# Kernel tuning notes

Measured on AMD Instinct MI355X. Metric: run time of the kernel, lower is better.

The kernel has to match this reference:

```python
import jax, jax.numpy as jnp
import numpy as np

D = 512       # d_model
H = 8         # n_heads per pathway MHA
CTX_H = 2     # router context_attention heads
P = 16        # num_attention_pathways
K = 8         # top_k_pathways
B = 8
S = 1024
TEMP = 1.0
RH1, RH2 = 128, 64  # router hidden sizes


def mha(x, in_w, in_b, out_w, out_b, n_heads):
    """torch.nn.MultiheadAttention (batch_first, eval mode, no mask)."""
    b, s, d = x.shape
    dh = d // n_heads
    qkv = x @ in_w.T + in_b                      # [b,s,3d]
    q, k, v = jnp.split(qkv, 3, axis=-1)
    sh = lambda t: t.reshape(b, s, n_heads, dh).transpose(0, 2, 1, 3)
    q, k, v = sh(q), sh(k), sh(v)
    scale = 1.0 / float(np.sqrt(dh))
    attn = jax.nn.softmax(jnp.einsum('bhqd,bhkd->bhqk', q, k) * scale, axis=-1)
    o = jnp.einsum('bhqk,bhkd->bhqd', attn, v).transpose(0, 2, 1, 3).reshape(b, s, d)
    return o @ out_w.T + out_b


def setup_inputs() -> dict:
    key = jax.random.key(0)
    ks = jax.random.split(key, 16)
    w = 0.05  # weight init scale to keep attention logits sane
    return {
        'x': jax.random.normal(ks[0], (B, S, D), jnp.float32),
        'ctx_in_w': jax.random.normal(ks[1], (3 * D, D), jnp.float32) * w,
        'ctx_in_b': jnp.zeros((3 * D,), jnp.float32),
        'ctx_out_w': jax.random.normal(ks[2], (D, D), jnp.float32) * w,
        'ctx_out_b': jnp.zeros((D,), jnp.float32),
        'r_w1': jax.random.normal(ks[3], (RH1, D), jnp.float32) * w,
        'r_b1': jnp.zeros((RH1,), jnp.float32),
        'r_w2': jax.random.normal(ks[4], (RH2, RH1), jnp.float32) * w,
        'r_b2': jnp.zeros((RH2,), jnp.float32),
        'r_w3': jax.random.normal(ks[5], (P, RH2), jnp.float32) * w,
        'r_b3': jnp.zeros((P,), jnp.float32),
        'p_in_w': jax.random.normal(ks[6], (P, 3 * D, D), jnp.float32) * w,
        'p_in_b': jnp.zeros((P, 3 * D), jnp.float32),
        'p_out_w': jax.random.normal(ks[7], (P, D, D), jnp.float32) * w,
        'p_out_b': jnp.zeros((P, D), jnp.float32),
    }


def reference(x, ctx_in_w, ctx_in_b, ctx_out_w, ctx_out_b,
              r_w1, r_b1, r_w2, r_b2, r_w3, r_b3,
              p_in_w, p_in_b, p_out_w, p_out_b):
    b, s, d = x.shape
    # --- SemanticPathwayRouter ---
    attended = mha(x, ctx_in_w, ctx_in_b, ctx_out_w, ctx_out_b, CTX_H)
    h = jax.nn.relu(attended @ r_w1.T + r_b1)
    h = jax.nn.relu(h @ r_w2.T + r_b2)
    pathway_scores = h @ r_w3.T + r_b3            # [b,s,P]
    # --- GLBL load-balance loss (eval: no buffer updates) ---
    probs_lb = jax.nn.softmax(pathway_scores, axis=-1)
    freq = probs_lb.mean(axis=(0, 1))             # [P] (frequencies == avg scores)
    glbl_loss = P * jnp.sum(freq * freq)
    # --- top-k gating: softmax -> topk scatter -> renormalize ---
    probs = jax.nn.softmax(pathway_scores / TEMP, axis=-1)
    top_v, top_i = jax.lax.top_k(probs, K)        # [b,s,K]
    bi = jnp.arange(b)[:, None, None]
    si = jnp.arange(s)[None, :, None]
    weights = jnp.zeros_like(probs).at[bi, si, top_i].set(top_v)
    weights = weights / (weights.sum(axis=-1, keepdims=True) + 1e-8)
    # --- combine: weighted sum of P full-MHA experts (scan keeps memory low) ---
    wp = jnp.moveaxis(weights, -1, 0)             # [P,b,s]
    def step(acc, params):
        iw, ib, ow, ob, wk = params
        return acc + mha(x, iw, ib, ow, ob, H) * wk[..., None], None
    output, _ = jax.lax.scan(step, jnp.zeros_like(x),
                             (p_in_w, p_in_b, p_out_w, p_out_b, wp))
    return output, glbl_loss, weights
```

## Files before the change

kernel.cpp:

```cpp
#include <hip/hip_runtime.h>
#include <math.h>

#define TOKENS 8192
#define DM 512
#define TD 1536
#define SEQ 1024
#define NPATH 16
#define TOPK 8

typedef __bf16 bf16x8v __attribute__((ext_vector_type(8)));
typedef __bf16 bf16x4v __attribute__((ext_vector_type(4)));
typedef float f32x4v __attribute__((ext_vector_type(4)));

__device__ __forceinline__ void gload_lds16(const void* gp, unsigned lds_byte_off) {
    __builtin_amdgcn_global_load_lds(
        (const __attribute__((address_space(1))) unsigned int*)(uintptr_t)gp,
        (__attribute__((address_space(3))) unsigned int*)(uintptr_t)lds_byte_off,
        16, 0, 0);
}

__global__ __launch_bounds__(256)
void gemm_f32_nt(const float* __restrict__ A, const float* __restrict__ B,
                 const float* __restrict__ bias, float* __restrict__ C,
                 int M, int N, int K, int lda, int ldb, int ldc,
                 float alpha, int relu, int zmode)
{
    __shared__ float As[16][132];
    __shared__ float Bs[16][132];
    if (zmode == 1) {
        const int z = blockIdx.z, bb = z >> 1, hh = z & 1;
        A += (size_t)bb * SEQ * TD + hh * 256;
        B += (size_t)bb * SEQ * TD + 512 + hh * 256;
        C += (size_t)z * SEQ * SEQ;
    }
    const int tid = threadIdx.x;
    const int bm = blockIdx.y << 7, bn = blockIdx.x << 7;
    const int tx4 = (tid & 15) << 2, ty4 = ((tid >> 4) & 15) << 2;
    float acc[8][8] = {};
    for (int k0 = 0; k0 < K; k0 += 16) {
        __syncthreads();
#pragma unroll
        for (int it = 0; it < 2; ++it) {
            const int u = (it << 8) + tid;
            const int row = u >> 2, kc4 = (u & 3) << 2;
            const float4 av = *(const float4*)(A + (size_t)(bm + row) * lda + k0 + kc4);
            As[kc4 + 0][row] = av.x; As[kc4 + 1][row] = av.y;
            As[kc4 + 2][row] = av.z; As[kc4 + 3][row] = av.w;
            const float4 bv = *(const float4*)(B + (size_t)(bn + row) * ldb + k0 + kc4);
            Bs[kc4 + 0][row] = bv.x; Bs[kc4 + 1][row] = bv.y;
            Bs[kc4 + 2][row] = bv.z; Bs[kc4 + 3][row] = bv.w;
        }
        __syncthreads();
#pragma unroll
        for (int kk = 0; kk < 16; ++kk) {
            const float4 a0 = *(const float4*)&As[kk][ty4];
            const float4 a1 = *(const float4*)&As[kk][64 + ty4];
            const float4 b0 = *(const float4*)&Bs[kk][tx4];
            const float4 b1 = *(const float4*)&Bs[kk][64 + tx4];
            const float aa[8] = {a0.x, a0.y, a0.z, a0.w, a1.x, a1.y, a1.z, a1.w};
            const float bb[8] = {b0.x, b0.y, b0.z, b0.w, b1.x, b1.y, b1.z, b1.w};
#pragma unroll
            for (int i = 0; i < 8; ++i)
#pragma unroll
                for (int j = 0; j < 8; ++j)
                    acc[i][j] = fmaf(aa[i], bb[j], acc[i][j]);
        }
    }
    float bcol[8] = {};
    if (bias) {
        const float4 bL = *(const float4*)(bias + bn + tx4);
        const float4 bH = *(const float4*)(bias + bn + 64 + tx4);
        bcol[0] = bL.x; bcol[1] = bL.y; bcol[2] = bL.z; bcol[3] = bL.w;
        bcol[4] = bH.x; bcol[5] = bH.y; bcol[6] = bH.z; bcol[7] = bH.w;
    }
#pragma unroll
    for (int i = 0; i < 8; ++i) {
        const int row = bm + ((i < 4) ? (ty4 + i) : (64 + ty4 + i - 4));
        float* cp = C + (size_t)row * ldc + bn;
        float v[8];
#pragma unroll
        for (int j = 0; j < 8; ++j) {
            v[j] = alpha * acc[i][j] + bcol[j];
            if (relu) v[j] = fmaxf(v[j], 0.f);
        }
        *(float4*)(cp + tx4) = make_float4(v[0], v[1], v[2], v[3]);
        *(float4*)(cp + 64 + tx4) = make_float4(v[4], v[5], v[6], v[7]);
    }
}

__global__ __launch_bounds__(256)
void gemm_f32_pv(const float* __restrict__ Sb, const float* __restrict__ qkv,
                 float* __restrict__ obuf)
{
    __shared__ float As[16][132];
    __shared__ float Bs[16][128];
    const int z = blockIdx.z, bb = z >> 1, hh = z & 1;
    const float* A = Sb + (size_t)z * SEQ * SEQ;
    const float* B = qkv + (size_t)bb * SEQ * TD + 1024 + hh * 256;
    float* C = obuf + (size_t)bb * SEQ * 512 + hh * 256;
    const int tid = threadIdx.x;
    const int bm = blockIdx.y << 7, bn = blockIdx.x << 7;
    const int tx4 = (tid & 15) << 2, ty4 = ((tid >> 4) & 15) << 2;
    float acc[8][8] = {};
    for (int k0 = 0; k0 < SEQ; k0 += 16) {
        __syncthreads();
#pragma unroll
        for (int it = 0; it < 2; ++it) {
            const int u = (it << 8) + tid;
            const int row = u >> 2, kc4 = (u & 3) << 2;
            const float4 av = *(const float4*)(A + (size_t)(bm + row) * SEQ + k0 + kc4);
            As[kc4 + 0][row] = av.x; As[kc4 + 1][row] = av.y;
            As[kc4 + 2][row] = av.z; As[kc4 + 3][row] = av.w;
            const int krow = u >> 5, n4 = (u & 31) << 2;
            *(float4*)&Bs[krow][n4] = *(const float4*)(B + (size_t)(k0 + krow) * TD + bn + n4);
        }
        __syncthreads();
#pragma unroll
        for (int kk = 0; kk < 16; ++kk) {
            const float4 a0 = *(const float4*)&As[kk][ty4];
            const float4 a1 = *(const float4*)&As[kk][64 + ty4];
            const float4 b0 = *(const float4*)&Bs[kk][tx4];
            const float4 b1 = *(const float4*)&Bs[kk][64 + tx4];
            const float aa[8] = {a0.x, a0.y, a0.z, a0.w, a1.x, a1.y, a1.z, a1.w};
            const float bb[8] = {b0.x, b0.y, b0.z, b0.w, b1.x, b1.y, b1.z, b1.w};
#pragma unroll
            for (int i = 0; i < 8; ++i)
#pragma unroll
                for (int j = 0; j < 8; ++j)
                    acc[i][j] = fmaf(aa[i], bb[j], acc[i][j]);
        }
    }
#pragma unroll
    for (int i = 0; i < 8; ++i) {
        const int row = bm + ((i < 4) ? (ty4 + i) : (64 + ty4 + i - 4));
        float* cp = C + (size_t)row * 512 + bn;
        *(float4*)(cp + tx4) = make_float4(acc[i][0], acc[i][1], acc[i][2], acc[i][3]);
        *(float4*)(cp + 64 + tx4) = make_float4(acc[i][4], acc[i][5], acc[i][6], acc[i][7]);
    }
}

__global__ __launch_bounds__(256)
void softmax_rows(float* __restrict__ S_)
{
    const int row = blockIdx.x * 4 + (threadIdx.x >> 6);
    const int lane = threadIdx.x & 63;
    float* rp = S_ + (size_t)row * 1024 + lane * 16;
    float4 v[4];
#pragma unroll
    for (int i = 0; i < 4; ++i) v[i] = *(const float4*)(rp + i * 4);
    float mx = -INFINITY;
#pragma unroll
    for (int i = 0; i < 4; ++i)
        mx = fmaxf(mx, fmaxf(fmaxf(v[i].x, v[i].y), fmaxf(v[i].z, v[i].w)));
#pragma unroll
    for (int off = 1; off < 64; off <<= 1) mx = fmaxf(mx, __shfl_xor(mx, off));
    float sum = 0.f;
#pragma unroll
    for (int i = 0; i < 4; ++i) {
        v[i].x = __expf(v[i].x - mx); v[i].y = __expf(v[i].y - mx);
        v[i].z = __expf(v[i].z - mx); v[i].w = __expf(v[i].w - mx);
        sum += v[i].x + v[i].y + v[i].z + v[i].w;
    }
#pragma unroll
    for (int off = 1; off < 64; off <<= 1) sum += __shfl_xor(sum, off);
    const float inv = 1.f / sum;
#pragma unroll
    for (int i = 0; i < 4; ++i) {
        v[i].x *= inv; v[i].y *= inv; v[i].z *= inv; v[i].w *= inv;
        *(float4*)(rp + i * 4) = v[i];
    }
}

__global__ __launch_bounds__(256)
void gemm_f32(const float* __restrict__ A, const float* __restrict__ W,
              const float* __restrict__ bias, float* __restrict__ C,
              int M, int N, int K, int relu)
{
    __shared__ float As[16][64];
    __shared__ float Bs[16][64];
    const int bm = blockIdx.y << 6;
    const int bn = blockIdx.x << 6;
    const int tid = threadIdx.x;
    const int tx = tid & 15, ty = tid >> 4;
    const int lr = tid >> 2;
    const int lc = (tid & 3) << 2;
    float acc[4][4] = {};
    for (int k0 = 0; k0 < K; k0 += 16) {
        float4 av = *(const float4*)(A + (size_t)(bm + lr) * K + (k0 + lc));
        float4 bv = make_float4(0.f, 0.f, 0.f, 0.f);
        const int wr = bn + lr;
        if (wr < N) bv = *(const float4*)(W + (size_t)wr * K + (k0 + lc));
        __syncthreads();
        As[lc + 0][lr] = av.x; As[lc + 1][lr] = av.y;
        As[lc + 2][lr] = av.z; As[lc + 3][lr] = av.w;
        Bs[lc + 0][lr] = bv.x; Bs[lc + 1][lr] = bv.y;
        Bs[lc + 2][lr] = bv.z; Bs[lc + 3][lr] = bv.w;
        __syncthreads();
#pragma unroll
        for (int kk = 0; kk < 16; ++kk) {
            const float4 a4 = *(const float4*)(&As[kk][ty << 2]);
            const float4 b4 = *(const float4*)(&Bs[kk][tx << 2]);
            const float a[4] = {a4.x, a4.y, a4.z, a4.w};
            const float b[4] = {b4.x, b4.y, b4.z, b4.w};
#pragma unroll
            for (int i = 0; i < 4; ++i)
#pragma unroll
                for (int j = 0; j < 4; ++j)
                    acc[i][j] = fmaf(a[i], b[j], acc[i][j]);
        }
    }
#pragma unroll
    for (int i = 0; i < 4; ++i) {
        const int m = bm + (ty << 2) + i;
#pragma unroll
        for (int j = 0; j < 4; ++j) {
            const int n = bn + (tx << 2) + j;
            if (n < N) {
                float v = acc[i][j] + bias[n];
                if (relu) v = fmaxf(v, 0.f);
                C[(size_t)m * N + n] = v;
            }
        }
    }
}

template <int DH>
__global__ __launch_bounds__(256)
void flash_attn(const float* __restrict__ qkv, float* __restrict__ O,
                int H, float scale)
{
    constexpr int NU = DH / 64;
    __shared__ float Qs[32][DH + 4];
    __shared__ float Ks[32][DH + 4];
    __shared__ float Vs[32][DH + 4];
    __shared__ float Ps[32][33];
    const int tid = threadIdx.x;
    const int g2 = tid & 15;
    const int rs = tid >> 4;
    const int bh = blockIdx.y;
    const int b = bh / H, h = bh - b * H;
    const int rb = blockIdx.x << 5;
    const float* qb = qkv + (size_t)b * SEQ * TD + (size_t)h * DH;
    const float* kb = qb + DM;
    const float* vb = qb + 2 * DM;

    for (int idx = tid; idx < 32 * (DH / 4); idx += 256) {
        const int rr = idx / (DH / 4);
        const int dp = (idx - rr * (DH / 4)) << 2;
        float4 v = *(const float4*)(qb + (size_t)(rb + rr) * TD + dp);
        v.x *= scale; v.y *= scale; v.z *= scale; v.w *= scale;
        *(float4*)&Qs[rr][dp] = v;
    }
    float m0 = -INFINITY, m1 = -INFINITY, l0 = 0.f, l1 = 0.f;
    float4 o0[NU], o1[NU];
#pragma unroll
    for (int u = 0; u < NU; ++u) {
        o0[u] = make_float4(0.f, 0.f, 0.f, 0.f);
        o1[u] = make_float4(0.f, 0.f, 0.f, 0.f);
    }
    __syncthreads();

    for (int kt = 0; kt < SEQ; kt += 32) {
        for (int idx = tid; idx < 32 * (DH / 4); idx += 256) {
            const int rr = idx / (DH / 4);
            const int dp = (idx - rr * (DH / 4)) << 2;
            *(float4*)&Ks[rr][dp] = *(const float4*)(kb + (size_t)(kt + rr) * TD + dp);
            *(float4*)&Vs[rr][dp] = *(const float4*)(vb + (size_t)(kt + rr) * TD + dp);
        }
        __syncthreads();
        float s00 = 0.f, s01 = 0.f, s10 = 0.f, s11 = 0.f;
        const int cA = g2, cB = g2 + 16;
#pragma unroll 8
        for (int i = 0; i < DH; i += 4) {
            const float4 q0 = *(const float4*)&Qs[rs][i];
            const float4 q1 = *(const float4*)&Qs[rs + 16][i];
            const float4 k0 = *(const float4*)&Ks[cA][i];
            const float4 k1 = *(const float4*)&Ks[cB][i];
            s00 += q0.x * k0.x + q0.y * k0.y + q0.z * k0.z + q0.w * k0.w;
            s01 += q0.x * k1.x + q0.y * k1.y + q0.z * k1.z + q0.w * k1.w;
            s10 += q1.x * k0.x + q1.y * k0.y + q1.z * k0.z + q1.w * k0.w;
            s11 += q1.x * k1.x + q1.y * k1.y + q1.z * k1.z + q1.w * k1.w;
        }
        float ml0 = fmaxf(s00, s01), ml1 = fmaxf(s10, s11);
#pragma unroll
        for (int off = 1; off < 16; off <<= 1) {
            ml0 = fmaxf(ml0, __shfl_xor(ml0, off));
            ml1 = fmaxf(ml1, __shfl_xor(ml1, off));
        }
        const float n0 = fmaxf(m0, ml0), n1 = fmaxf(m1, ml1);
        const float f0 = __expf(m0 - n0), f1 = __expf(m1 - n1);
        const float p00 = __expf(s00 - n0), p01 = __expf(s01 - n0);
        const float p10 = __expf(s10 - n1), p11 = __expf(s11 - n1);
        float sum0 = p00 + p01, sum1 = p10 + p11;
#pragma unroll
        for (int off = 1; off < 16; off <<= 1) {
            sum0 += __shfl_xor(sum0, off);
            sum1 += __shfl_xor(sum1, off);
        }
        l0 = l0 * f0 + sum0; l1 = l1 * f1 + sum1;
        m0 = n0; m1 = n1;
#pragma unroll
        for (int u = 0; u < NU; ++u) {
            o0[u].x *= f0; o0[u].y *= f0; o0[u].z *= f0; o0[u].w *= f0;
            o1[u].x *= f1; o1[u].y *= f1; o1[u].z *= f1; o1[u].w *= f1;
        }
        Ps[rs][cA] = p00; Ps[rs][cB] = p01;
        Ps[rs + 16][cA] = p10; Ps[rs + 16][cB] = p11;
        __syncthreads();
#pragma unroll 4
        for (int c = 0; c < 32; ++c) {
            const float pv0 = Ps[rs][c];
            const float pv1 = Ps[rs + 16][c];
#pragma unroll
            for (int u = 0; u < NU; ++u) {
                const float4 v4 = *(const float4*)&Vs[c][(g2 << 2) + (u << 6)];
                o0[u].x = fmaf(pv0, v4.x, o0[u].x);
                o0[u].y = fmaf(pv0, v4.y, o0[u].y);
                o0[u].z = fmaf(pv0, v4.z, o0[u].z);
                o0[u].w = fmaf(pv0, v4.w, o0[u].w);
                o1[u].x = fmaf(pv1, v4.x, o1[u].x);
                o1[u].y = fmaf(pv1, v4.y, o1[u].y);
                o1[u].z = fmaf(pv1, v4.z, o1[u].z);
                o1[u].w = fmaf(pv1, v4.w, o1[u].w);
            }
        }
        __syncthreads();
    }
    const float i0 = 1.f / l0, i1 = 1.f / l1;
    float* ob0 = O + (size_t)b * SEQ * DM + (size_t)(rb + rs) * DM + h * DH;
    float* ob1 = ob0 + (size_t)16 * DM;
#pragma unroll
    for (int u = 0; u < NU; ++u) {
        float4 w0 = o0[u];
        w0.x *= i0; w0.y *= i0; w0.z *= i0; w0.w *= i0;
        *(float4*)(ob0 + (g2 << 2) + (u << 6)) = w0;
        float4 w1 = o1[u];
        w1.x *= i1; w1.y *= i1; w1.z *= i1; w1.w *= i1;
        *(float4*)(ob1 + (g2 << 2) + (u << 6)) = w1;
    }
}

__global__ __launch_bounds__(256)
void router_epilogue(const float* __restrict__ scores, float* __restrict__ freq,
                     float* __restrict__ weights)
{
    const int t = blockIdx.x * 256 + threadIdx.x;
    float s[NPATH];
#pragma unroll
    for (int i = 0; i < NPATH; ++i) s[i] = scores[(size_t)t * NPATH + i];
    float mx = s[0];
#pragma unroll
    for (int i = 1; i < NPATH; ++i) mx = fmaxf(mx, s[i]);
    float p[NPATH];
    float sum = 0.f;
#pragma unroll
    for (int i = 0; i < NPATH; ++i) { p[i] = expf(s[i] - mx); sum += p[i]; }
    const float inv = 1.f / sum;
#pragma unroll
    for (int i = 0; i < NPATH; ++i) p[i] *= inv;
#pragma unroll
    for (int i = 0; i < NPATH; ++i) {
        float v = p[i];
        for (int off = 32; off >= 1; off >>= 1) v += __shfl_xor(v, off);
        if ((threadIdx.x & 63) == 0) atomicAdd(&freq[i], v);
    }
    unsigned used = 0u;
    float topv[TOPK];
    int topi[TOPK];
    float wsum = 0.f;
#pragma unroll
    for (int k = 0; k < TOPK; ++k) {
        float best = -1.f; int bi = 0;
#pragma unroll
        for (int i = 0; i < NPATH; ++i) {
            if (!((used >> i) & 1u) && p[i] > best) { best = p[i]; bi = i; }
        }
        used |= 1u << bi;
        topv[k] = best; topi[k] = bi;
        wsum += best;
    }
    const float winv = 1.f / (wsum + 1e-8f);
    float w[NPATH];
#pragma unroll
    for (int i = 0; i < NPATH; ++i) w[i] = 0.f;
#pragma unroll
    for (int k = 0; k < TOPK; ++k) w[topi[k]] = topv[k] * winv;
#pragma unroll
    for (int i = 0; i < NPATH; ++i) weights[(size_t)t * NPATH + i] = w[i];
}

__global__ void glbl_loss_kernel(const float* __restrict__ freq, float* __restrict__ out)
{
    if (threadIdx.x == 0 && blockIdx.x == 0) {
        float acc = 0.f;
        for (int i = 0; i < NPATH; ++i) {
            const float f = freq[i] * (1.f / (float)TOKENS);
            acc += f * f;
        }
        out[0] = (float)NPATH * acc;
    }
}

__global__ __launch_bounds__(256)
void cast_f32_bf16(const float* __restrict__ src, __bf16* __restrict__ dst, int n)
{
    const int i = (blockIdx.x * 256 + threadIdx.x) * 4;
    if (i < n) {
        const float4 v = *(const float4*)(src + i);
        bf16x4v o;
        o[0] = (__bf16)v.x; o[1] = (__bf16)v.y; o[2] = (__bf16)v.z; o[3] = (__bf16)v.w;
        *(bf16x4v*)(dst + i) = o;
    }
}

__global__ __launch_bounds__(256)
void gemm_bf16_qkv(const __bf16* __restrict__ A, const __bf16* __restrict__ B,
                   const float* __restrict__ bias, __bf16* __restrict__ C,
                   int N, int K)
{
    __shared__ __attribute__((aligned(16))) __bf16 As[128 * 32];
    __shared__ __attribute__((aligned(16))) __bf16 Bs[128 * 32];
    const int tid = threadIdx.x;
    const int l = tid & 63, w = tid >> 6;
    const int wr = w >> 1, wc = w & 1;
    const int a16 = l & 15, g = l >> 4;
    const int bm = blockIdx.y << 7, bn = blockIdx.x << 7;
    const unsigned asA = (unsigned)(uintptr_t)(void*)&As[0];
    const unsigned asB = (unsigned)(uintptr_t)(void*)&Bs[0];

    f32x4v acc[4][4] = {};
    for (int k0 = 0; k0 < K; k0 += 32) {
        __syncthreads();
#pragma unroll
        for (int it = 0; it < 2; ++it) {
            const int u = it * 256 + tid;
            const int row = u >> 2, cc = u & 3;
            const unsigned dst = (unsigned)((it * 256 + w * 64) * 16);
            gload_lds16(A + (size_t)(bm + row) * K + k0 + cc * 8, asA + dst);
            gload_lds16(B + (size_t)(bn + row) * K + k0 + cc * 8, asB + dst);
        }
        __syncthreads();
        bf16x8v af[4], bf[4];
#pragma unroll
        for (int m = 0; m < 4; ++m)
            af[m] = *(const bf16x8v*)&As[(wr * 64 + m * 16 + a16) * 32 + g * 8];
#pragma unroll
        for (int n = 0; n < 4; ++n)
            bf[n] = *(const bf16x8v*)&Bs[(wc * 64 + n * 16 + a16) * 32 + g * 8];
#pragma unroll
        for (int m = 0; m < 4; ++m)
#pragma unroll
            for (int n = 0; n < 4; ++n)
                acc[m][n] = __builtin_amdgcn_mfma_f32_16x16x32_bf16(af[m], bf[n], acc[m][n], 0, 0, 0);
    }
#pragma unroll
    for (int n = 0; n < 4; ++n) {
        const int col = bn + wc * 64 + n * 16 + a16;
        const float bv = bias[col];
        const float sc = (col < DM) ? 0.125f : 1.0f;
#pragma unroll
        for (int m = 0; m < 4; ++m) {
            const int row0 = bm + wr * 64 + m * 16 + g * 4;
#pragma unroll
            for (int r = 0; r < 4; ++r)
                C[(size_t)(row0 + r) * N + col] = (__bf16)((acc[m][n][r] + bv) * sc);
        }
    }
}

__global__ __launch_bounds__(256)
void gemm_bf16_out(const __bf16* __restrict__ A, const __bf16* __restrict__ B,
                   const float* __restrict__ bias, const float* __restrict__ wts,
                   float* __restrict__ out, int path, int first)
{
    __shared__ __attribute__((aligned(16))) __bf16 As[128 * 32];
    __shared__ __attribute__((aligned(16))) __bf16 Bs[128 * 32];
    const int tid = threadIdx.x;
    const int l = tid & 63, w = tid >> 6;
    const int wr = w >> 1, wc = w & 1;
    const int a16 = l & 15, g = l >> 4;
    const int bm = blockIdx.y << 7, bn = blockIdx.x << 7;
    const unsigned asA = (unsigned)(uintptr_t)(void*)&As[0];
    const unsigned asB = (unsigned)(uintptr_t)(void*)&Bs[0];

    f32x4v acc[4][4] = {};
    for (int k0 = 0; k0 < DM; k0 += 32) {
        __syncthreads();
#pragma unroll
        for (int it = 0; it < 2; ++it) {
            const int u = it * 256 + tid;
            const int row = u >> 2, cc = u & 3;
            const unsigned dst = (unsigned)((it * 256 + w * 64) * 16);
            gload_lds16(A + (size_t)(bm + row) * DM + k0 + cc * 8, asA + dst);
            gload_lds16(B + (size_t)(bn + row) * DM + k0 + cc * 8, asB + dst);
        }
        __syncthreads();
        bf16x8v af[4], bf[4];
#pragma unroll
        for (int m = 0; m < 4; ++m)
            af[m] = *(const bf16x8v*)&As[(wr * 64 + m * 16 + a16) * 32 + g * 8];
#pragma unroll
        for (int n = 0; n < 4; ++n)
            bf[n] = *(const bf16x8v*)&Bs[(wc * 64 + n * 16 + a16) * 32 + g * 8];
#pragma unroll
        for (int m = 0; m < 4; ++m)
#pragma unroll
            for (int n = 0; n < 4; ++n)
                acc[m][n] = __builtin_amdgcn_mfma_f32_16x16x32_bf16(af[m], bf[n], acc[m][n], 0, 0, 0);
    }
#pragma unroll
    for (int m = 0; m < 4; ++m) {
        const int row0 = bm + wr * 64 + m * 16 + g * 4;
#pragma unroll
        for (int r = 0; r < 4; ++r) {
            const int row = row0 + r;
            const float wk = wts[(size_t)row * NPATH + path];
#pragma unroll
            for (int n = 0; n < 4; ++n) {
                const int col = bn + wc * 64 + n * 16 + a16;
                const float v = (acc[m][n][r] + bias[col]) * wk;
                const size_t oi = (size_t)row * DM + col;
                if (first) out[oi] = v; else out[oi] += v;
            }
        }
    }
}

__global__ __launch_bounds__(256)
void attn_bf16(const __bf16* __restrict__ qkv, __bf16* __restrict__ O)
{
    __shared__ __attribute__((aligned(16))) __bf16 Ks[64 * 72];
    __shared__ __attribute__((aligned(16))) __bf16 Vt[64 * 72];
    __shared__ __attribute__((aligned(16))) __bf16 Pq[4][16 * 72];
    const int tid = threadIdx.x;
    const int l = tid & 63, w = tid >> 6;
    const int a = l & 15, g = l >> 4;
    const int bh = blockIdx.y;
    const int b = bh >> 3, h = bh & 7;
    const int qb = blockIdx.x << 6;
    const size_t base = (size_t)b * SEQ * TD;

    bf16x8v qf[2];
    {
        const int qrow = qb + w * 16 + a;
        const __bf16* qp = qkv + base + (size_t)qrow * TD + h * 64 + g * 8;
        qf[0] = *(const bf16x8v*)qp;
        qf[1] = *(const bf16x8v*)(qp + 32);
    }
    float m_ = -INFINITY, l_ = 0.f;
    f32x4v o_[4] = {};
    __bf16* pw = &Pq[w][0];

    for (int kt = 0; kt < SEQ; kt += 64) {
#pragma unroll
        for (int it = 0; it < 2; ++it) {
            const int u = it * 256 + tid;
            const int kr = u >> 3, c8 = u & 7;
            const __bf16* kp = qkv + base + (size_t)(kt + kr) * TD + DM + h * 64 + c8 * 8;
            const bf16x8v kv = *(const bf16x8v*)kp;
            *(bf16x8v*)&Ks[kr * 72 + c8 * 8] = kv;
            const bf16x8v vv = *(const bf16x8v*)(kp + DM);
            const int swzg = ((kr >> 3) ^ c8) & 7;
#pragma unroll
            for (int j = 0; j < 8; ++j)
                Vt[(c8 * 8 + j) * 72 + swzg * 8 + (kr & 7)] = vv[j];
        }
        __syncthreads();

        f32x4v s[4] = {};
#pragma unroll
        for (int kc = 0; kc < 4; ++kc) {
            const bf16x8v kf0 = *(const bf16x8v*)&Ks[(kc * 16 + a) * 72 + g * 8];
            const bf16x8v kf1 = *(const bf16x8v*)&Ks[(kc * 16 + a) * 72 + 32 + g * 8];
            s[kc] = __builtin_amdgcn_mfma_f32_16x16x32_bf16(kf0, qf[0], s[kc], 0, 0, 0);
            s[kc] = __builtin_amdgcn_mfma_f32_16x16x32_bf16(kf1, qf[1], s[kc], 0, 0, 0);
        }

        float pmax = s[0][0];
#pragma unroll
        for (int kc = 0; kc < 4; ++kc)
#pragma unroll
            for (int r = 0; r < 4; ++r) pmax = fmaxf(pmax, s[kc][r]);
        pmax = fmaxf(pmax, __shfl_xor(pmax, 16));
        pmax = fmaxf(pmax, __shfl_xor(pmax, 32));

        if (__any(pmax > m_ + 8.f)) {
            const float nm = fmaxf(m_, pmax);
            const float f = __expf(m_ - nm);
            m_ = nm;
            l_ *= f;
#pragma unroll
            for (int r = 0; r < 4; ++r) {
                const float fr = __shfl(f, 4 * g + r);
#pragma unroll
                for (int dc = 0; dc < 4; ++dc) o_[dc][r] *= fr;
            }
        }
        float p[4][4];
        float lsum = 0.f;
#pragma unroll
        for (int kc = 0; kc < 4; ++kc)
#pragma unroll
            for (int r = 0; r < 4; ++r) {
                p[kc][r] = __expf(s[kc][r] - m_);
                lsum += p[kc][r];
            }
        lsum += __shfl_xor(lsum, 16);
        lsum += __shfl_xor(lsum, 32);
        l_ += lsum;

#pragma unroll
        for (int kc = 0; kc < 4; ++kc) {
            bf16x4v pk;
            pk[0] = (__bf16)p[kc][0]; pk[1] = (__bf16)p[kc][1];
            pk[2] = (__bf16)p[kc][2]; pk[3] = (__bf16)p[kc][3];
            *(bf16x4v*)&pw[a * 72 + kc * 16 + g * 4] = pk;
        }
        asm volatile("s_waitcnt lgkmcnt(0)" ::: "memory");

#pragma unroll
        for (int dc = 0; dc < 4; ++dc) {
            const int vrow = dc * 16 + a;
#pragma unroll
            for (int kh = 0; kh < 2; ++kh) {
                const bf16x8v pa = *(const bf16x8v*)&pw[a * 72 + kh * 32 + g * 8];
                const bf16x8v vf = *(const bf16x8v*)&Vt[vrow * 72 + ((((kh << 2) + g) ^ ((vrow >> 3) & 7)) & 7) * 8];
                o_[dc] = __builtin_amdgcn_mfma_f32_16x16x32_bf16(pa, vf, o_[dc], 0, 0, 0);
            }
        }
        __syncthreads();
    }

    float linv[4];
#pragma unroll
    for (int r = 0; r < 4; ++r) linv[r] = 1.f / __shfl(l_, 4 * g + r);
    const int row0 = qb + w * 16 + g * 4;
#pragma unroll
    for (int dc = 0; dc < 4; ++dc)
#pragma unroll
        for (int r = 0; r < 4; ++r)
            O[(size_t)(b * SEQ + row0 + r) * DM + h * 64 + dc * 16 + a] = (__bf16)(o_[dc][r] * linv[r]);
}

extern "C" void kernel_launch(void* const* d_in, const int* in_sizes, int n_in,
                              void* d_out, int out_size, void* d_ws, size_t ws_size,
                              hipStream_t stream)
{
    const float* x         = (const float*)d_in[0];
    const float* ctx_in_w  = (const float*)d_in[1];
    const float* ctx_in_b  = (const float*)d_in[2];
    const float* ctx_out_w = (const float*)d_in[3];
    const float* ctx_out_b = (const float*)d_in[4];
    const float* r_w1      = (const float*)d_in[5];
    const float* r_b1      = (const float*)d_in[6];
    const float* r_w2      = (const float*)d_in[7];
    const float* r_b2      = (const float*)d_in[8];
    const float* r_w3      = (const float*)d_in[9];
    const float* r_b3      = (const float*)d_in[10];
    const float* p_in_w    = (const float*)d_in[11];
    const float* p_in_b    = (const float*)d_in[12];
    const float* p_out_w   = (const float*)d_in[13];
    const float* p_out_b   = (const float*)d_in[14];

    float* out  = (float*)d_out;
    float* loss = out + (size_t)TOKENS * DM;
    float* wts  = loss + 1;

    float* F = (float*)d_ws;
    float* qkvbuf   = F;
    float* obuf     = F + 12582912;
    float* attended = F;
    float* h1       = F + 4194304;
    float* h2       = F + 5242880;
    float* scores   = F + 5767168;
    float* freq     = F + 5898240;

    const int M = TOKENS;
    dim3 blk(256);
    const bool big = ws_size >= (size_t)134217728;

    hipMemsetAsync(freq, 0, NPATH * sizeof(float), stream);
    gemm_f32_nt<<<dim3(TD / 128, M / 128), blk, 0, stream>>>(
        x, ctx_in_w, ctx_in_b, qkvbuf, M, TD, DM, DM, DM, TD, 1.f, 0, 0);
    if (big) {
        float* Sbuf = F + 16777216;
        gemm_f32_nt<<<dim3(8, 8, 16), blk, 0, stream>>>(
            qkvbuf, qkvbuf, nullptr, Sbuf, SEQ, SEQ, 256, TD, TD, SEQ, 0.0625f, 0, 1);
        softmax_rows<<<dim3(16 * SEQ / 4), blk, 0, stream>>>(Sbuf);
        gemm_f32_pv<<<dim3(2, 8, 16), blk, 0, stream>>>(Sbuf, qkvbuf, obuf);
    } else {
        flash_attn<256><<<dim3(SEQ / 32, 8 * 2), blk, 0, stream>>>(qkvbuf, obuf, 2, 1.f / 16.f);
    }
    gemm_f32_nt<<<dim3(DM / 128, M / 128), blk, 0, stream>>>(
        obuf, ctx_out_w, ctx_out_b, attended, M, DM, DM, DM, DM, DM, 1.f, 0, 0);
    gemm_f32_nt<<<dim3(1, M / 128), blk, 0, stream>>>(
        attended, r_w1, r_b1, h1, M, 128, DM, DM, DM, 128, 1.f, 1, 0);
    gemm_f32<<<dim3(1, M / 64), blk, 0, stream>>>(h1, r_w2, r_b2, h2, M, 64, 128, 1);
    gemm_f32<<<dim3(1, M / 64), blk, 0, stream>>>(h2, r_w3, r_b3, scores, M, NPATH, 64, 0);
    router_epilogue<<<dim3(TOKENS / 256), blk, 0, stream>>>(scores, freq, wts);
    glbl_loss_kernel<<<dim3(1), dim3(64), 0, stream>>>(freq, loss);

    if (big) {
        __bf16* xb       = (__bf16*)F;
        __bf16* qkv_b    = (__bf16*)(F + 2097152);
        __bf16* obuf_b   = (__bf16*)(F + 8388608);
        __bf16* wqkv_all = (__bf16*)(F + 10485760);
        __bf16* wout_all = (__bf16*)(F + 16777216);
        cast_f32_bf16<<<dim3(TOKENS * DM / 4 / 256), blk, 0, stream>>>(x, xb, TOKENS * DM);
        cast_f32_bf16<<<dim3(NPATH * TD * DM / 4 / 256), blk, 0, stream>>>(
            p_in_w, wqkv_all, NPATH * TD * DM);
        cast_f32_bf16<<<dim3(NPATH * DM * DM / 4 / 256), blk, 0, stream>>>(
            p_out_w, wout_all, NPATH * DM * DM);
        for (int p = 0; p < NPATH; ++p) {
            gemm_bf16_qkv<<<dim3(TD / 128, M / 128), blk, 0, stream>>>(
                xb, wqkv_all + (size_t)p * TD * DM, p_in_b + (size_t)p * TD, qkv_b, TD, DM);
            attn_bf16<<<dim3(SEQ / 64, 64), blk, 0, stream>>>(qkv_b, obuf_b);
            gemm_bf16_out<<<dim3(DM / 128, M / 128), blk, 0, stream>>>(
                obuf_b, wout_all + (size_t)p * DM * DM, p_out_b + (size_t)p * DM, wts, out, p, p == 0);
        }
    } else {
        __bf16* xb     = (__bf16*)F;
        __bf16* qkv_b  = (__bf16*)(F + 6000000);
        __bf16* obuf_b = (__bf16*)(F + 12582912);
        __bf16* wqkv_b = (__bf16*)(F + 12582912 + 2100000);
        __bf16* wout_b = (__bf16*)(F + 12582912 + 2500000);
        cast_f32_bf16<<<dim3(TOKENS * DM / 4 / 256), blk, 0, stream>>>(x, xb, TOKENS * DM);
        for (int p = 0; p < NPATH; ++p) {
            cast_f32_bf16<<<dim3(TD * DM / 4 / 256), blk, 0, stream>>>(
                p_in_w + (size_t)p * TD * DM, wqkv_b, TD * DM);
            cast_f32_bf16<<<dim3(DM * DM / 4 / 256), blk, 0, stream>>>(
                p_out_w + (size_t)p * DM * DM, wout_b, DM * DM);
            gemm_bf16_qkv<<<dim3(TD / 128, M / 128), blk, 0, stream>>>(
                xb, wqkv_b, p_in_b + (size_t)p * TD, qkv_b, TD, DM);
            attn_bf16<<<dim3(SEQ / 64, 64), blk, 0, stream>>>(qkv_b, obuf_b);
            gemm_bf16_out<<<dim3(DM / 128, M / 128), blk, 0, stream>>>(
                obuf_b, wout_b, p_out_b + (size_t)p * DM, wts, out, p, p == 0);
        }
    }
}
```

Before: 2.358 ms.

## Write V transposed from QKV GEMM and load K/V fragments directly from global

The QKV GEMM epilogue now writes V into a separate per-(batch,head) transposed buffer, so the attention kernel can load K and V MFMA fragments straight from global memory into registers. This removes the LDS staging, the scalar transpose scatter into LDS and both block-wide barriers per key tile. The attention grid is also remapped to a 1D launch that groups query blocks of the same batch/head, and s_setprio is raised around the MFMA sections. The trade-offs are uncoalesced scattered stores of V in the GEMM epilogue, redundant global loads of K/V by each wave (relying on cache), and moved workspace offsets.

```diff
diff --git a/kernel.cpp b/kernel.cpp
--- a/kernel.cpp
+++ b/kernel.cpp
@@ -416,7 +416,7 @@
 __global__ __launch_bounds__(256)
 void gemm_bf16_qkv(const __bf16* __restrict__ A, const __bf16* __restrict__ B,
                    const float* __restrict__ bias, __bf16* __restrict__ C,
-                   int N, int K)
+                   __bf16* __restrict__ vT, int N, int K)
 {
     __shared__ __attribute__((aligned(16))) __bf16 As[128 * 32];
     __shared__ __attribute__((aligned(16))) __bf16 Bs[128 * 32];
@@ -457,13 +457,26 @@
     for (int n = 0; n < 4; ++n) {
         const int col = bn + wc * 64 + n * 16 + a16;
         const float bv = bias[col];
-        const float sc = (col < DM) ? 0.125f : 1.0f;
-#pragma unroll
-        for (int m = 0; m < 4; ++m) {
-            const int row0 = bm + wr * 64 + m * 16 + g * 4;
-#pragma unroll
-            for (int r = 0; r < 4; ++r)
-                C[(size_t)(row0 + r) * N + col] = (__bf16)((acc[m][n][r] + bv) * sc);
+        if (col < 1024) {
+            const float sc = (col < DM) ? 0.125f : 1.0f;
+#pragma unroll
+            for (int m = 0; m < 4; ++m) {
+                const int row0 = bm + wr * 64 + m * 16 + g * 4;
+#pragma unroll
+                for (int r = 0; r < 4; ++r)
+                    C[(size_t)(row0 + r) * N + col] = (__bf16)((acc[m][n][r] + bv) * sc);
+            }
+        } else {
+#pragma unroll
+            for (int m = 0; m < 4; ++m) {
+                const int row0 = bm + wr * 64 + m * 16 + g * 4;
+#pragma unroll
+                for (int r = 0; r < 4; ++r) {
+                    const int row = row0 + r;
+                    vT[((size_t)(row >> 10) * 512 + (col - 1024)) * SEQ + (row & 1023)] =
+                        (__bf16)(acc[m][n][r] + bv);
+                }
+            }
         }
     }
 }
@@ -527,17 +540,18 @@
 }
 
 __global__ __launch_bounds__(256)
-void attn_bf16(const __bf16* __restrict__ qkv, __bf16* __restrict__ O)
-{
-    __shared__ __attribute__((aligned(16))) __bf16 Ks[64 * 72];
-    __shared__ __attribute__((aligned(16))) __bf16 Vt[64 * 72];
+void attn_bf16(const __bf16* __restrict__ qkv, const __bf16* __restrict__ vT,
+               __bf16* __restrict__ O)
+{
     __shared__ __attribute__((aligned(16))) __bf16 Pq[4][16 * 72];
     const int tid = threadIdx.x;
     const int l = tid & 63, w = tid >> 6;
     const int a = l & 15, g = l >> 4;
-    const int bh = blockIdx.y;
+    const int i = blockIdx.x;
+    const int k = i >> 3;
+    const int bh = (i & 7) + ((k >> 4) << 3);
+    const int qb = (k & 15) << 6;
     const int b = bh >> 3, h = bh & 7;
-    const int qb = blockIdx.x << 6;
     const size_t base = (size_t)b * SEQ * TD;
 
     bf16x8v qf[2];
@@ -547,34 +561,36 @@
         qf[0] = *(const bf16x8v*)qp;
         qf[1] = *(const bf16x8v*)(qp + 32);
     }
+    const __bf16* Kg = qkv + base + (size_t)a * TD + DM + h * 64 + g * 8;
+    const __bf16* Vg = vT + ((size_t)bh * 64 + a) * SEQ + g * 8;
+
     float m_ = -INFINITY, l_ = 0.f;
     f32x4v o_[4] = {};
     __bf16* pw = &Pq[w][0];
 
     for (int kt = 0; kt < SEQ; kt += 64) {
-#pragma unroll
-        for (int it = 0; it < 2; ++it) {
-            const int u = it * 256 + tid;
-            const int kr = u >> 3, c8 = u & 7;
-            const __bf16* kp = qkv + base + (size_t)(kt + kr) * TD + DM + h * 64 + c8 * 8;
-            const bf16x8v kv = *(const bf16x8v*)kp;
-            *(bf16x8v*)&Ks[kr * 72 + c8 * 8] = kv;
-            const bf16x8v vv = *(const bf16x8v*)(kp + DM);
-            const int swzg = ((kr >> 3) ^ c8) & 7;
-#pragma unroll
-            for (int j = 0; j < 8; ++j)
-                Vt[(c8 * 8 + j) * 72 + swzg * 8 + (kr & 7)] = vv[j];
-        }
-        __syncthreads();
-
+        const __bf16* kp = Kg + (size_t)kt * TD;
+        bf16x8v kf0[4], kf1[4];
+#pragma unroll
+        for (int kc = 0; kc < 4; ++kc) {
+            kf0[kc] = *(const bf16x8v*)(kp + (size_t)(kc * 16) * TD);
+            kf1[kc] = *(const bf16x8v*)(kp + (size_t)(kc * 16) * TD + 32);
+        }
+        bf16x8v vf[4][2];
+        const __bf16* vp = Vg + kt;
+#pragma unroll
+        for (int dc = 0; dc < 4; ++dc) {
+            vf[dc][0] = *(const bf16x8v*)(vp + (size_t)(dc * 16) * SEQ);
+            vf[dc][1] = *(const bf16x8v*)(vp + (size_t)(dc * 16) * SEQ + 32);
+        }
         f32x4v s[4] = {};
+        __builtin_amdgcn_s_setprio(1);
 #pragma unroll
         for (int kc = 0; kc < 4; ++kc) {
-            const bf16x8v kf0 = *(const bf16x8v*)&Ks[(kc * 16 + a) * 72 + g * 8];
-            const bf16x8v kf1 = *(const bf16x8v*)&Ks[(kc * 16 + a) * 72 + 32 + g * 8];
-            s[kc] = __builtin_amdgcn_mfma_f32_16x16x32_bf16(kf0, qf[0], s[kc], 0, 0, 0);
-            s[kc] = __builtin_amdgcn_mfma_f32_16x16x32_bf16(kf1, qf[1], s[kc], 0, 0, 0);
-        }
+            s[kc] = __builtin_amdgcn_mfma_f32_16x16x32_bf16(kf0[kc], qf[0], s[kc], 0, 0, 0);
+            s[kc] = __builtin_amdgcn_mfma_f32_16x16x32_bf16(kf1[kc], qf[1], s[kc], 0, 0, 0);
+        }
+        __builtin_amdgcn_s_setprio(0);
 
         float pmax = s[0][0];
 #pragma unroll
@@ -617,18 +633,16 @@
             *(bf16x4v*)&pw[a * 72 + kc * 16 + g * 4] = pk;
         }
         asm volatile("s_waitcnt lgkmcnt(0)" ::: "memory");
-
+        const bf16x8v pa0 = *(const bf16x8v*)&pw[a * 72 + g * 8];
+        const bf16x8v pa1 = *(const bf16x8v*)&pw[a * 72 + 32 + g * 8];
+
+        __builtin_amdgcn_s_setprio(1);
 #pragma unroll
         for (int dc = 0; dc < 4; ++dc) {
-            const int vrow = dc * 16 + a;
-#pragma unroll
-            for (int kh = 0; kh < 2; ++kh) {
-                const bf16x8v pa = *(const bf16x8v*)&pw[a * 72 + kh * 32 + g * 8];
-                const bf16x8v vf = *(const bf16x8v*)&Vt[vrow * 72 + ((((kh << 2) + g) ^ ((vrow >> 3) & 7)) & 7) * 8];
-                o_[dc] = __builtin_amdgcn_mfma_f32_16x16x32_bf16(pa, vf, o_[dc], 0, 0, 0);
-            }
-        }
-        __syncthreads();
+            o_[dc] = __builtin_amdgcn_mfma_f32_16x16x32_bf16(pa0, vf[dc][0], o_[dc], 0, 0, 0);
+            o_[dc] = __builtin_amdgcn_mfma_f32_16x16x32_bf16(pa1, vf[dc][1], o_[dc], 0, 0, 0);
+        }
+        __builtin_amdgcn_s_setprio(0);
     }
 
     float linv[4];
@@ -674,6 +688,10 @@
     float* h2       = F + 5242880;
     float* scores   = F + 5767168;
     float* freq     = F + 5898240;
+    __bf16* xb     = (__bf16*)F;
+    __bf16* qkv_b  = (__bf16*)(F + 2097152);
+    __bf16* obuf_b = (__bf16*)(F + 8388608);
+    __bf16* vT_b   = (__bf16*)(F + 10485760);
 
     const int M = TOKENS;
     dim3 blk(256);
@@ -700,39 +718,32 @@
     router_epilogue<<<dim3(TOKENS / 256), blk, 0, stream>>>(scores, freq, wts);
     glbl_loss_kernel<<<dim3(1), dim3(64), 0, stream>>>(freq, loss);
 
+    cast_f32_bf16<<<dim3(TOKENS * DM / 4 / 256), blk, 0, stream>>>(x, xb, TOKENS * DM);
     if (big) {
-        __bf16* xb       = (__bf16*)F;
-        __bf16* qkv_b    = (__bf16*)(F + 2097152);
-        __bf16* obuf_b   = (__bf16*)(F + 8388608);
-        __bf16* wqkv_all = (__bf16*)(F + 10485760);
-        __bf16* wout_all = (__bf16*)(F + 16777216);
-        cast_f32_bf16<<<dim3(TOKENS * DM / 4 / 256), blk, 0, stream>>>(x, xb, TOKENS * DM);
+        __bf16* wqkv_all = (__bf16*)(F + 16777216);
+        __bf16* wout_all = (__bf16*)(F + 23068672);
         cast_f32_bf16<<<dim3(NPATH * TD * DM / 4 / 256), blk, 0, stream>>>(
             p_in_w, wqkv_all, NPATH * TD * DM);
         cast_f32_bf16<<<dim3(NPATH * DM * DM / 4 / 256), blk, 0, stream>>>(
             p_out_w, wout_all, NPATH * DM * DM);
         for (int p = 0; p < NPATH; ++p) {
             gemm_bf16_qkv<<<dim3(TD / 128, M / 128), blk, 0, stream>>>(
-                xb, wqkv_all + (size_t)p * TD * DM, p_in_b + (size_t)p * TD, qkv_b, TD, DM);
-            attn_bf16<<<dim3(SEQ / 64, 64), blk, 0, stream>>>(qkv_b, obuf_b);
+                xb, wqkv_all + (size_t)p * TD * DM, p_in_b + (size_t)p * TD, qkv_b, vT_b, TD, DM);
+            attn_bf16<<<dim3(1024), blk, 0, stream>>>(qkv_b, vT_b, obuf_b);
             gemm_bf16_out<<<dim3(DM / 128, M / 128), blk, 0, stream>>>(
                 obuf_b, wout_all + (size_t)p * DM * DM, p_out_b + (size_t)p * DM, wts, out, p, p == 0);
         }
     } else {
-        __bf16* xb     = (__bf16*)F;
-        __bf16* qkv_b  = (__bf16*)(F + 6000000);
-        __bf16* obuf_b = (__bf16*)(F + 12582912);
-        __bf16* wqkv_b = (__bf16*)(F + 12582912 + 2100000);
-        __bf16* wout_b = (__bf16*)(F + 12582912 + 2500000);
-        cast_f32_bf16<<<dim3(TOKENS * DM / 4 / 256), blk, 0, stream>>>(x, xb, TOKENS * DM);
+        __bf16* wqkv_b = (__bf16*)(F + 12582912);
+        __bf16* wout_b = (__bf16*)(F + 12976128);
         for (int p = 0; p < NPATH; ++p) {
             cast_f32_bf16<<<dim3(TD * DM / 4 / 256), blk, 0, stream>>>(
                 p_in_w + (size_t)p * TD * DM, wqkv_b, TD * DM);
             cast_f32_bf16<<<dim3(DM * DM / 4 / 256), blk, 0, stream>>>(
                 p_out_w + (size_t)p * DM * DM, wout_b, DM * DM);
             gemm_bf16_qkv<<<dim3(TD / 128, M / 128), blk, 0, stream>>>(
-                xb, wqkv_b, p_in_b + (size_t)p * TD, qkv_b, TD, DM);
-            attn_bf16<<<dim3(SEQ / 64, 64), blk, 0, stream>>>(qkv_b, obuf_b);
+                xb, wqkv_b, p_in_b + (size_t)p * TD, qkv_b, vT_b, TD, DM);
+            attn_bf16<<<dim3(1024), blk, 0, stream>>>(qkv_b, vT_b, obuf_b);
             gemm_bf16_out<<<dim3(DM / 128, M / 128), blk, 0, stream>>>(
                 obuf_b, wout_b, p_out_b + (size_t)p * DM, wts, out, p, p == 0);
         }
```

After: 3.499 ms. +48.4%, slower.

## Process two query tiles per wave in bf16 attention to reuse K/V loads

Applied to the files above, without the earlier changes.

Each wave in the bf16 attention kernel now handles 32 query rows (two 16-row tiles) instead of 16, so each block covers 128 queries and loads each K/V tile from global once per 128 queries rather than once per 64. The V transpose store is rewritten to pack pairs of rows into 32-bit LDS writes, and s_setprio is raised around the MFMA sections. Workspace offsets are also reshuffled. This halves the grid to 512 blocks per pathway and doubles accumulator register use, which may reduce occupancy and parallelism.

```diff
diff --git a/kernel.cpp b/kernel.cpp
--- a/kernel.cpp
+++ b/kernel.cpp
@@ -11,6 +11,7 @@
 typedef __bf16 bf16x8v __attribute__((ext_vector_type(8)));
 typedef __bf16 bf16x4v __attribute__((ext_vector_type(4)));
 typedef float f32x4v __attribute__((ext_vector_type(4)));
+typedef unsigned short u16x8 __attribute__((ext_vector_type(8)));
 
 __device__ __forceinline__ void gload_lds16(const void* gp, unsigned lds_byte_off) {
     __builtin_amdgcn_global_load_lds(
@@ -531,25 +532,30 @@
 {
     __shared__ __attribute__((aligned(16))) __bf16 Ks[64 * 72];
     __shared__ __attribute__((aligned(16))) __bf16 Vt[64 * 72];
-    __shared__ __attribute__((aligned(16))) __bf16 Pq[4][16 * 72];
+    __shared__ __attribute__((aligned(16))) __bf16 Pq[4][32 * 72];
     const int tid = threadIdx.x;
     const int l = tid & 63, w = tid >> 6;
     const int a = l & 15, g = l >> 4;
     const int bh = blockIdx.y;
     const int b = bh >> 3, h = bh & 7;
-    const int qb = blockIdx.x << 6;
+    const int qb = blockIdx.x << 7;
     const size_t base = (size_t)b * SEQ * TD;
 
-    bf16x8v qf[2];
+    bf16x8v qA0, qA1, qB0, qB1;
     {
-        const int qrow = qb + w * 16 + a;
-        const __bf16* qp = qkv + base + (size_t)qrow * TD + h * 64 + g * 8;
-        qf[0] = *(const bf16x8v*)qp;
-        qf[1] = *(const bf16x8v*)(qp + 32);
-    }
-    float m_ = -INFINITY, l_ = 0.f;
-    f32x4v o_[4] = {};
+        const __bf16* qp = qkv + base + (size_t)(qb + w * 32 + a) * TD + h * 64 + g * 8;
+        qA0 = *(const bf16x8v*)qp;
+        qA1 = *(const bf16x8v*)(qp + 32);
+        const __bf16* qp2 = qp + (size_t)16 * TD;
+        qB0 = *(const bf16x8v*)qp2;
+        qB1 = *(const bf16x8v*)(qp2 + 32);
+    }
+    float mA = -INFINITY, lA = 0.f, mB = -INFINITY, lB = 0.f;
+    f32x4v oA[4] = {}, oB[4] = {};
     __bf16* pw = &Pq[w][0];
+    const int c8v = tid & 7;
+    const int pr  = tid >> 3;
+    const int vcol8 = (pr >> 2) ^ c8v;
 
     for (int kt = 0; kt < SEQ; kt += 64) {
 #pragma unroll
@@ -557,89 +563,136 @@
             const int u = it * 256 + tid;
             const int kr = u >> 3, c8 = u & 7;
             const __bf16* kp = qkv + base + (size_t)(kt + kr) * TD + DM + h * 64 + c8 * 8;
-            const bf16x8v kv = *(const bf16x8v*)kp;
-            *(bf16x8v*)&Ks[kr * 72 + c8 * 8] = kv;
-            const bf16x8v vv = *(const bf16x8v*)(kp + DM);
-            const int swzg = ((kr >> 3) ^ c8) & 7;
-#pragma unroll
-            for (int j = 0; j < 8; ++j)
-                Vt[(c8 * 8 + j) * 72 + swzg * 8 + (kr & 7)] = vv[j];
-        }
-        __syncthreads();
-
-        f32x4v s[4] = {};
+            *(bf16x8v*)&Ks[kr * 72 + c8 * 8] = *(const bf16x8v*)kp;
+        }
+        {
+            const __bf16* vp = qkv + base + (size_t)(kt + 2 * pr) * TD + 2 * DM + h * 64 + c8v * 8;
+            const u16x8 v0 = __builtin_bit_cast(u16x8, *(const bf16x8v*)vp);
+            const u16x8 v1 = __builtin_bit_cast(u16x8, *(const bf16x8v*)(vp + TD));
+#pragma unroll
+            for (int j = 0; j < 8; ++j) {
+                const unsigned pk = (unsigned)v0[j] | ((unsigned)v1[j] << 16);
+                *(unsigned*)&Vt[(c8v * 8 + j) * 72 + vcol8 * 8 + (pr & 3) * 2] = pk;
+            }
+        }
+        __syncthreads();
+
+        f32x4v sA[4] = {}, sB[4] = {};
+        __builtin_amdgcn_s_setprio(1);
 #pragma unroll
         for (int kc = 0; kc < 4; ++kc) {
             const bf16x8v kf0 = *(const bf16x8v*)&Ks[(kc * 16 + a) * 72 + g * 8];
             const bf16x8v kf1 = *(const bf16x8v*)&Ks[(kc * 16 + a) * 72 + 32 + g * 8];
-            s[kc] = __builtin_amdgcn_mfma_f32_16x16x32_bf16(kf0, qf[0], s[kc], 0, 0, 0);
-            s[kc] = __builtin_amdgcn_mfma_f32_16x16x32_bf16(kf1, qf[1], s[kc], 0, 0, 0);
-        }
-
-        float pmax = s[0][0];
-#pragma unroll
-        for (int kc = 0; kc < 4; ++kc)
-#pragma unroll
-            for (int r = 0; r < 4; ++r) pmax = fmaxf(pmax, s[kc][r]);
-        pmax = fmaxf(pmax, __shfl_xor(pmax, 16));
-        pmax = fmaxf(pmax, __shfl_xor(pmax, 32));
-
-        if (__any(pmax > m_ + 8.f)) {
-            const float nm = fmaxf(m_, pmax);
-            const float f = __expf(m_ - nm);
-            m_ = nm;
-            l_ *= f;
-#pragma unroll
-            for (int r = 0; r < 4; ++r) {
-                const float fr = __shfl(f, 4 * g + r);
-#pragma unroll
-                for (int dc = 0; dc < 4; ++dc) o_[dc][r] *= fr;
-            }
-        }
-        float p[4][4];
-        float lsum = 0.f;
-#pragma unroll
-        for (int kc = 0; kc < 4; ++kc)
-#pragma unroll
-            for (int r = 0; r < 4; ++r) {
-                p[kc][r] = __expf(s[kc][r] - m_);
-                lsum += p[kc][r];
-            }
-        lsum += __shfl_xor(lsum, 16);
-        lsum += __shfl_xor(lsum, 32);
-        l_ += lsum;
-
-#pragma unroll
-        for (int kc = 0; kc < 4; ++kc) {
-            bf16x4v pk;
-            pk[0] = (__bf16)p[kc][0]; pk[1] = (__bf16)p[kc][1];
-            pk[2] = (__bf16)p[kc][2]; pk[3] = (__bf16)p[kc][3];
-            *(bf16x4v*)&pw[a * 72 + kc * 16 + g * 4] = pk;
+            sA[kc] = __builtin_amdgcn_mfma_f32_16x16x32_bf16(kf0, qA0, sA[kc], 0, 0, 0);
+            sA[kc] = __builtin_amdgcn_mfma_f32_16x16x32_bf16(kf1, qA1, sA[kc], 0, 0, 0);
+            sB[kc] = __builtin_amdgcn_mfma_f32_16x16x32_bf16(kf0, qB0, sB[kc], 0, 0, 0);
+            sB[kc] = __builtin_amdgcn_mfma_f32_16x16x32_bf16(kf1, qB1, sB[kc], 0, 0, 0);
+        }
+        __builtin_amdgcn_s_setprio(0);
+
+        {
+            float pmax = sA[0][0];
+#pragma unroll
+            for (int kc = 0; kc < 4; ++kc)
+#pragma unroll
+                for (int r = 0; r < 4; ++r) pmax = fmaxf(pmax, sA[kc][r]);
+            pmax = fmaxf(pmax, __shfl_xor(pmax, 16));
+            pmax = fmaxf(pmax, __shfl_xor(pmax, 32));
+            if (__any(pmax > mA + 8.f)) {
+                const float nm = fmaxf(mA, pmax);
+                const float f = __expf(mA - nm);
+                mA = nm; lA *= f;
+#pragma unroll
+                for (int r = 0; r < 4; ++r) {
+                    const float fr = __shfl(f, 4 * g + r);
+#pragma unroll
+                    for (int dc = 0; dc < 4; ++dc) oA[dc][r] *= fr;
+                }
+            }
+            float lsum = 0.f;
+#pragma unroll
+            for (int kc = 0; kc < 4; ++kc) {
+                bf16x4v pk;
+#pragma unroll
+                for (int r = 0; r < 4; ++r) {
+                    const float pv = __expf(sA[kc][r] - mA);
+                    lsum += pv;
+                    pk[r] = (__bf16)pv;
+                }
+                *(bf16x4v*)&pw[a * 72 + kc * 16 + g * 4] = pk;
+            }
+            lsum += __shfl_xor(lsum, 16);
+            lsum += __shfl_xor(lsum, 32);
+            lA += lsum;
+        }
+        {
+            float pmax = sB[0][0];
+#pragma unroll
+            for (int kc = 0; kc < 4; ++kc)
+#pragma unroll
+                for (int r = 0; r < 4; ++r) pmax = fmaxf(pmax, sB[kc][r]);
+            pmax = fmaxf(pmax, __shfl_xor(pmax, 16));
+            pmax = fmaxf(pmax, __shfl_xor(pmax, 32));
+            if (__any(pmax > mB + 8.f)) {
+                const float nm = fmaxf(mB, pmax);
+                const float f = __expf(mB - nm);
+                mB = nm; lB *= f;
+#pragma unroll
+                for (int r = 0; r < 4; ++r) {
+                    const float fr = __shfl(f, 4 * g + r);
+#pragma unroll
+                    for (int dc = 0; dc < 4; ++dc) oB[dc][r] *= fr;
+                }
+            }
+            float lsum = 0.f;
+#pragma unroll
+            for (int kc = 0; kc < 4; ++kc) {
+                bf16x4v pk;
+#pragma unroll
+                for (int r = 0; r < 4; ++r) {
+                    const float pv = __expf(sB[kc][r] - mB);
+                    lsum += pv;
+                    pk[r] = (__bf16)pv;
+                }
+                *(bf16x4v*)&pw[(16 + a) * 72 + kc * 16 + g * 4] = pk;
+            }
+            lsum += __shfl_xor(lsum, 16);
+            lsum += __shfl_xor(lsum, 32);
+            lB += lsum;
         }
         asm volatile("s_waitcnt lgkmcnt(0)" ::: "memory");
 
+        __builtin_amdgcn_s_setprio(1);
 #pragma unroll
         for (int dc = 0; dc < 4; ++dc) {
             const int vrow = dc * 16 + a;
 #pragma unroll
             for (int kh = 0; kh < 2; ++kh) {
-                const bf16x8v pa = *(const bf16x8v*)&pw[a * 72 + kh * 32 + g * 8];
                 const bf16x8v vf = *(const bf16x8v*)&Vt[vrow * 72 + ((((kh << 2) + g) ^ ((vrow >> 3) & 7)) & 7) * 8];
-                o_[dc] = __builtin_amdgcn_mfma_f32_16x16x32_bf16(pa, vf, o_[dc], 0, 0, 0);
-            }
-        }
-        __syncthreads();
-    }
-
-    float linv[4];
-#pragma unroll
-    for (int r = 0; r < 4; ++r) linv[r] = 1.f / __shfl(l_, 4 * g + r);
-    const int row0 = qb + w * 16 + g * 4;
+                const bf16x8v paA = *(const bf16x8v*)&pw[a * 72 + kh * 32 + g * 8];
+                const bf16x8v paB = *(const bf16x8v*)&pw[(16 + a) * 72 + kh * 32 + g * 8];
+                oA[dc] = __builtin_amdgcn_mfma_f32_16x16x32_bf16(paA, vf, oA[dc], 0, 0, 0);
+                oB[dc] = __builtin_amdgcn_mfma_f32_16x16x32_bf16(paB, vf, oB[dc], 0, 0, 0);
+            }
+        }
+        __builtin_amdgcn_s_setprio(0);
+        __syncthreads();
+    }
+
+    float liA[4], liB[4];
+#pragma unroll
+    for (int r = 0; r < 4; ++r) {
+        liA[r] = 1.f / __shfl(lA, 4 * g + r);
+        liB[r] = 1.f / __shfl(lB, 4 * g + r);
+    }
+    const int row0 = qb + w * 32 + g * 4;
 #pragma unroll
     for (int dc = 0; dc < 4; ++dc)
 #pragma unroll
-        for (int r = 0; r < 4; ++r)
-            O[(size_t)(b * SEQ + row0 + r) * DM + h * 64 + dc * 16 + a] = (__bf16)(o_[dc][r] * linv[r]);
+        for (int r = 0; r < 4; ++r) {
+            O[(size_t)(b * SEQ + row0 + r) * DM + h * 64 + dc * 16 + a] = (__bf16)(oA[dc][r] * liA[r]);
+            O[(size_t)(b * SEQ + row0 + 16 + r) * DM + h * 64 + dc * 16 + a] = (__bf16)(oB[dc][r] * liB[r]);
+        }
 }
 
 extern "C" void kernel_launch(void* const* d_in, const int* in_sizes, int n_in,
@@ -704,8 +757,8 @@
         __bf16* xb       = (__bf16*)F;
         __bf16* qkv_b    = (__bf16*)(F + 2097152);
         __bf16* obuf_b   = (__bf16*)(F + 8388608);
-        __bf16* wqkv_all = (__bf16*)(F + 10485760);
-        __bf16* wout_all = (__bf16*)(F + 16777216);
+        __bf16* wqkv_all = (__bf16*)(F + 16777216);
+        __bf16* wout_all = (__bf16*)(F + 23068672);
         cast_f32_bf16<<<dim3(TOKENS * DM / 4 / 256), blk, 0, stream>>>(x, xb, TOKENS * DM);
         cast_f32_bf16<<<dim3(NPATH * TD * DM / 4 / 256), blk, 0, stream>>>(
             p_in_w, wqkv_all, NPATH * TD * DM);
@@ -714,16 +767,16 @@
         for (int p = 0; p < NPATH; ++p) {
             gemm_bf16_qkv<<<dim3(TD / 128, M / 128), blk, 0, stream>>>(
                 xb, wqkv_all + (size_t)p * TD * DM, p_in_b + (size_t)p * TD, qkv_b, TD, DM);
-            attn_bf16<<<dim3(SEQ / 64, 64), blk, 0, stream>>>(qkv_b, obuf_b);
+            attn_bf16<<<dim3(SEQ / 128, 64), blk, 0, stream>>>(qkv_b, obuf_b);
             gemm_bf16_out<<<dim3(DM / 128, M / 128), blk, 0, stream>>>(
                 obuf_b, wout_all + (size_t)p * DM * DM, p_out_b + (size_t)p * DM, wts, out, p, p == 0);
         }
     } else {
         __bf16* xb     = (__bf16*)F;
-        __bf16* qkv_b  = (__bf16*)(F + 6000000);
-        __bf16* obuf_b = (__bf16*)(F + 12582912);
-        __bf16* wqkv_b = (__bf16*)(F + 12582912 + 2100000);
-        __bf16* wout_b = (__bf16*)(F + 12582912 + 2500000);
+        __bf16* qkv_b  = (__bf16*)(F + 2097152);
+        __bf16* obuf_b = (__bf16*)(F + 8388608);
+        __bf16* wqkv_b = (__bf16*)(F + 12582912);
+        __bf16* wout_b = (__bf16*)(F + 12976128);
         cast_f32_bf16<<<dim3(TOKENS * DM / 4 / 256), blk, 0, stream>>>(x, xb, TOKENS * DM);
         for (int p = 0; p < NPATH; ++p) {
             cast_f32_bf16<<<dim3(TD * DM / 4 / 256), blk, 0, stream>>>(
@@ -732,7 +785,7 @@
                 p_out_w + (size_t)p * DM * DM, wout_b, DM * DM);
             gemm_bf16_qkv<<<dim3(TD / 128, M / 128), blk, 0, stream>>>(
                 xb, wqkv_b, p_in_b + (size_t)p * TD, qkv_b, TD, DM);
-            attn_bf16<<<dim3(SEQ / 64, 64), blk, 0, stream>>>(qkv_b, obuf_b);
+            attn_bf16<<<dim3(SEQ / 128, 64), blk, 0, stream>>>(qkv_b, obuf_b);
             gemm_bf16_out<<<dim3(DM / 128, M / 128), blk, 0, stream>>>(
                 obuf_b, wout_b, p_out_b + (size_t)p * DM, wts, out, p, p == 0);
         }
```

After: 2.298 ms. -2.5%, faster.
